# Optimization experiments

Hardware: AMD Instinct MI355X
Metric: run time of the kernel (lower is better)

Reference implementation:

```python
import jax, jax.numpy as jnp
import numpy as np

B, S, D_IN, D_EMB = 8, 2048, 512, 512

def setup_inputs() -> dict:
    key = jax.random.key(0)
    ks = jax.random.split(key, 7)
    s = 1.0 / np.sqrt(D_IN)
    return {
        "x": jax.random.normal(ks[0], (B, S, D_IN), dtype=jnp.float32),
        "Wq": jax.random.uniform(ks[1], (D_IN, D_EMB), jnp.float32, -s, s),
        "bq": jax.random.uniform(ks[2], (D_EMB,), jnp.float32, -s, s),
        "Wk": jax.random.uniform(ks[3], (D_IN, D_EMB), jnp.float32, -s, s),
        "bk": jax.random.uniform(ks[4], (D_EMB,), jnp.float32, -s, s),
        "Wv": jax.random.uniform(ks[5], (D_IN, D_EMB), jnp.float32, -s, s),
        "bv": jax.random.uniform(ks[6], (D_EMB,), jnp.float32, -s, s),
    }

def reference(x, Wq, bq, Wk, bk, Wv, bv):
    # single-head attention: softmax(QK^T / sqrt(d)) V
    q = x @ Wq + bq            # [B,S,E]
    k = x @ Wk + bk
    v = x @ Wv + bv
    scores = jnp.einsum('bse,bte->bst', q, k) / jnp.sqrt(jnp.float32(D_EMB))
    attn = jax.nn.softmax(scores, axis=-1)  # [B,S,S]
    return jnp.einsum('bst,bte->bse', attn, v)
```

## Files before the change

### kernel.cpp

```cpp
#include <hip/hip_runtime.h>
#include <stdint.h>


using f32x4 = __attribute__((ext_vector_type(4))) float;
using s16x8 = __attribute__((ext_vector_type(8))) short;
using u16x4 = __attribute__((ext_vector_type(4))) unsigned short;

#define S_LEN 2048
#define EMB   512

#define ASYNC16(g, l)                                                     \
  __builtin_amdgcn_global_load_lds(                                       \
      (const __attribute__((address_space(1))) void*)(g),                 \
      (__attribute__((address_space(3))) void*)(l), 16, 0, 0)

__device__ __forceinline__ unsigned short f2bf(float f) {
  union { float f; unsigned u; } v; v.f = f;
  unsigned r = v.u + 0x7fffu + ((v.u >> 16) & 1u);
  return (unsigned short)(r >> 16);
}

__global__ __launch_bounds__(256) void xconv_kernel(
    const float* __restrict__ x, short* __restrict__ xb) {
  int i = (blockIdx.x * 256 + threadIdx.x) * 8;
  f32x4 a = *(const f32x4*)(x + i);
  f32x4 b = *(const f32x4*)(x + i + 4);
  s16x8 h;
  h[0] = (short)f2bf(a[0]); h[1] = (short)f2bf(a[1]);
  h[2] = (short)f2bf(a[2]); h[3] = (short)f2bf(a[3]);
  h[4] = (short)f2bf(b[0]); h[5] = (short)f2bf(b[1]);
  h[6] = (short)f2bf(b[2]); h[7] = (short)f2bf(b[3]);
  *(s16x8*)(xb + i) = h;
}

__global__ __launch_bounds__(256) void wconv_kernel(
    const float* __restrict__ Wq, const float* __restrict__ Wk,
    const float* __restrict__ Wv, short* __restrict__ Wt) {
  __shared__ float T[64][65];
  int bid = blockIdx.x;
  int mat = bid >> 6;
  int t   = bid & 63;
  int k0  = (t & 7) << 6, n0 = (t >> 3) << 6;
  const float* W = (mat == 0) ? Wq : (mat == 1) ? Wk : Wv;
  int tid = threadIdx.x;
  int rr = tid >> 4, cc = tid & 15;
#pragma unroll
  for (int p = 0; p < 4; ++p) {
    int row = p * 16 + rr;
    f32x4 v = *(const f32x4*)(W + (size_t)(k0 + row) * 512 + n0 + cc * 4);
#pragma unroll
    for (int j = 0; j < 4; ++j) T[row][cc * 4 + j] = v[j];
  }
  __syncthreads();
  short* D = Wt + (size_t)mat * 262144;
#pragma unroll
  for (int p = 0; p < 4; ++p) {
    int nrow = p * 16 + rr;
    u16x4 h;
#pragma unroll
    for (int j = 0; j < 4; ++j) h[j] = f2bf(T[cc * 4 + j][nrow]);
    *(u16x4*)(D + (size_t)(n0 + nrow) * 512 + k0 + cc * 4) = h;
  }
}

__global__ __launch_bounds__(256) void qkv_gemm(
    const short* __restrict__ xb, const short* __restrict__ Wt,
    const float* __restrict__ bq, const float* __restrict__ bk,
    const float* __restrict__ bv,
    short* __restrict__ Qg, short* __restrict__ Kg, short* __restrict__ VTg) {
  __shared__ __align__(16) short As[2][128 * 64];
  __shared__ __align__(16) short Bs[2][128 * 64];
  int gid = blockIdx.x;
  int mat = gid >> 9;
  int rem = gid & 511;
  int mt  = rem & 127, nt = rem >> 7;
  int m0  = mt << 7,   n0 = nt << 7;
  const short* W    = Wt + (size_t)mat * 262144;
  const float* bias = (mat == 0) ? bq : (mat == 1) ? bk : bv;

  int tid = threadIdx.x, lane = tid & 63, wv = tid >> 6;
  int l16 = lane & 15, quad = lane >> 4;
  int wr = (wv & 1) << 6, wc = (wv >> 1) << 6;
  int drow = lane >> 3;
  int dchk = (lane & 7) ^ drow;

  const short* asrc[4];
  const short* bsrc[4];
#pragma unroll
  for (int i = 0; i < 4; ++i) {
    int row = (wv * 4 + i) * 8 + drow;
    asrc[i] = xb + (size_t)(m0 + row) * 512 + dchk * 8;
    bsrc[i] = W  + (size_t)(n0 + row) * 512 + dchk * 8;
  }

  const f32x4 Z4 = {0.f, 0.f, 0.f, 0.f};
  f32x4 acc[4][4];
#pragma unroll
  for (int a = 0; a < 4; ++a)
#pragma unroll
    for (int c = 0; c < 4; ++c) acc[a][c] = Z4;

#pragma unroll
  for (int i = 0; i < 4; ++i) {
    int g = wv * 4 + i;
    ASYNC16(asrc[i], &As[0][g * 512]);
    ASYNC16(bsrc[i], &Bs[0][g * 512]);
  }
  __syncthreads();

  for (int it = 0; it < 8; ++it) {
    int buf = it & 1;
    if (it < 7) {
      int k1 = (it + 1) << 6;
#pragma unroll
      for (int i = 0; i < 4; ++i) {
        int g = wv * 4 + i;
        ASYNC16(asrc[i] + k1, &As[buf ^ 1][g * 512]);
        ASYNC16(bsrc[i] + k1, &Bs[buf ^ 1][g * 512]);
      }
    }
#pragma unroll
    for (int kk = 0; kk < 2; ++kk) {
      s16x8 af[4], bfr[4];
#pragma unroll
      for (int rb = 0; rb < 4; ++rb) {
        int row = wr + rb * 16 + l16;
        int c   = kk * 4 + quad;
        af[rb] = *(const s16x8*)(&As[buf][row * 64 + ((c ^ (row & 7)) * 8)]);
      }
#pragma unroll
      for (int cb = 0; cb < 4; ++cb) {
        int row = wc + cb * 16 + l16;
        int c   = kk * 4 + quad;
        bfr[cb] = *(const s16x8*)(&Bs[buf][row * 64 + ((c ^ (row & 7)) * 8)]);
      }
#pragma unroll
      for (int rb = 0; rb < 4; ++rb)
#pragma unroll
        for (int cb = 0; cb < 4; ++cb)
          acc[rb][cb] = __builtin_amdgcn_mfma_f32_16x16x32_bf16(af[rb], bfr[cb], acc[rb][cb], 0, 0, 0);
    }
    __syncthreads();
  }

  float bsv[4];
#pragma unroll
  for (int cb = 0; cb < 4; ++cb) bsv[cb] = bias[n0 + wc + cb * 16 + l16];

  if (mat < 2) {
    short* D = (mat == 0) ? Qg : Kg;
#pragma unroll
    for (int rb = 0; rb < 4; ++rb)
#pragma unroll
      for (int cb = 0; cb < 4; ++cb)
#pragma unroll
        for (int r = 0; r < 4; ++r) {
          int m = m0 + wr + rb * 16 + quad * 4 + r;
          D[(size_t)m * 512 + n0 + wc + cb * 16 + l16] =
              (short)f2bf(acc[rb][cb][r] + bsv[cb]);
        }
  } else {
#pragma unroll
    for (int rb = 0; rb < 4; ++rb)
#pragma unroll
      for (int cb = 0; cb < 4; ++cb) {
        u16x4 h;
#pragma unroll
        for (int r = 0; r < 4; ++r) h[r] = f2bf(acc[rb][cb][r] + bsv[cb]);
        int m  = m0 + wr + rb * 16 + quad * 4;
        int bb = m >> 11, sl = m & 2047;
        int e  = n0 + wc + cb * 16 + l16;
        size_t idx = ((((size_t)bb * 32 + (e >> 4)) * 64 + (sl >> 5)) * 16 +
                      (e & 15)) * 32 + (sl & 31);
        *(u16x4*)(VTg + idx) = h;
      }
  }
}

__global__ __launch_bounds__(512, 2) void attn_kernel(
    const short* __restrict__ Qg, const short* __restrict__ Kg,
    const short* __restrict__ VTg, float* __restrict__ out) {
  __shared__ __align__(16) short Kt[3][32 * 512];
  __shared__ __align__(16) short Pl[2][64 * 40];
  __shared__ float l_l[64];
  const float SCL2 = 0.06375871855f;

  int b = blockIdx.x & 7, qt = blockIdx.x >> 3;
  int s0 = qt << 6;
  int tid = threadIdx.x, lane = tid & 63, wv = tid >> 6;
  int l16 = lane & 15, quad = lane >> 4;
  int a = wv & 3, h = wv >> 2;
  int e0 = wv << 6;

  const short* Kb = Kg  + (size_t)b * S_LEN * 512;
  const short* Vb = VTg + (size_t)b * 1048576;

  const short* kdma[4];
#pragma unroll
  for (int i = 0; i < 4; ++i) {
    int r = wv * 4 + i;
    kdma[i] = Kb + (size_t)r * 512 + ((lane ^ (r & 7)) * 8);
  }
  const short* vbase = Vb + (size_t)wv * 131072 + l16 * 32 + quad * 8;

#pragma unroll
  for (int i = 0; i < 4; ++i)
    ASYNC16(kdma[i], &Kt[0][(wv * 4 + i) * 512]);
#pragma unroll
  for (int i = 0; i < 4; ++i)
    ASYNC16(kdma[i] + 16384, &Kt[1][(wv * 4 + i) * 512]);

  const short* qrow = Qg + ((size_t)b * S_LEN + s0 + a * 16 + l16) * 512 + quad * 8;
  s16x8 qf[16];
#pragma unroll
  for (int kk = 0; kk < 16; ++kk) qf[kk] = *(const s16x8*)(qrow + kk * 32);

  const f32x4 Z4 = {0.f, 0.f, 0.f, 0.f};
  f32x4 acc[4][4];
#pragma unroll
  for (int rb = 0; rb < 4; ++rb)
#pragma unroll
    for (int cb = 0; cb < 4; ++cb) acc[rb][cb] = Z4;
  f32x4 lsum = Z4;

  __syncthreads();

  int rbuf = 0, wbuf = 2;
  for (int kt = 0; kt < 64; ++kt) {
    s16x8 vf[4];
#pragma unroll
    for (int cb = 0; cb < 4; ++cb)
      vf[cb] = *(const s16x8*)(vbase + (size_t)cb * 32768 + (size_t)kt * 512);
    __builtin_amdgcn_sched_barrier(0);

    {
      size_t adv = (size_t)((kt + 2) & 63) * 16384;
#pragma unroll
      for (int i = 0; i < 4; ++i)
        ASYNC16(kdma[i] + adv, &Kt[wbuf][(wv * 4 + i) * 512]);
    }
    __builtin_amdgcn_sched_barrier(0);

    f32x4 s_a = Z4, s_b = Z4;
    int krow = h * 16 + l16;
    const short* kb = &Kt[rbuf][krow * 512];
    int ksw = krow & 7;
    __builtin_amdgcn_s_setprio(1);
#pragma unroll
    for (int kk = 0; kk < 8; ++kk) {
      s16x8 kf0 = *(const s16x8*)(kb + (((2 * kk) * 4 + quad) ^ ksw) * 8);
      s_a = __builtin_amdgcn_mfma_f32_16x16x32_bf16(qf[2 * kk], kf0, s_a, 0, 0, 0);
      s16x8 kf1 = *(const s16x8*)(kb + (((2 * kk + 1) * 4 + quad) ^ ksw) * 8);
      s_b = __builtin_amdgcn_mfma_f32_16x16x32_bf16(qf[2 * kk + 1], kf1, s_b, 0, 0, 0);
    }
    __builtin_amdgcn_s_setprio(0);
    f32x4 sv = s_a + s_b;

    short* Pc = Pl[kt & 1];
#pragma unroll
    for (int r = 0; r < 4; ++r) {
      float p = exp2f(sv[r] * SCL2);
      lsum[r] += p;
      Pc[(a * 16 + quad * 4 + r) * 40 + h * 16 + l16] = (short)f2bf(p);
    }

    asm volatile("s_waitcnt vmcnt(8) lgkmcnt(0)\n\ts_barrier" ::: "memory");

    s16x8 pf[4];
#pragma unroll
    for (int g = 0; g < 4; ++g)
      pf[g] = *(const s16x8*)(Pc + (g * 16 + l16) * 40 + quad * 8);
    __builtin_amdgcn_s_setprio(1);
#pragma unroll
    for (int cb = 0; cb < 4; ++cb)
#pragma unroll
      for (int g = 0; g < 4; ++g)
        acc[g][cb] = __builtin_amdgcn_mfma_f32_16x16x32_bf16(pf[g], vf[cb], acc[g][cb], 0, 0, 0);
    __builtin_amdgcn_s_setprio(0);

    rbuf = (rbuf == 2) ? 0 : rbuf + 1;
    wbuf = (wbuf == 2) ? 0 : wbuf + 1;
  }

#pragma unroll
  for (int r = 0; r < 4; ++r) {
    float v = lsum[r];
    v += __shfl_xor(v, 1);
    v += __shfl_xor(v, 2);
    v += __shfl_xor(v, 4);
    v += __shfl_xor(v, 8);
    lsum[r] = v;
  }
  if (h == 0 && l16 == 0) {
#pragma unroll
    for (int r = 0; r < 4; ++r) l_l[a * 16 + quad * 4 + r] = lsum[r];
  }
  __syncthreads();
  if (h == 1 && l16 == 0) {
#pragma unroll
    for (int r = 0; r < 4; ++r) l_l[a * 16 + quad * 4 + r] += lsum[r];
  }
  __syncthreads();

#pragma unroll
  for (int rb = 0; rb < 4; ++rb) {
    f32x4 lv = *(const f32x4*)(l_l + rb * 16 + quad * 4);
    f32x4 li;
#pragma unroll
    for (int r = 0; r < 4; ++r) li[r] = 1.0f / lv[r];
#pragma unroll
    for (int cb = 0; cb < 4; ++cb)
#pragma unroll
      for (int r = 0; r < 4; ++r)
        out[((size_t)b * S_LEN + s0 + rb * 16 + quad * 4 + r) * 512 + e0 + cb * 16 + l16] =
            acc[rb][cb][r] * li[r];
  }
}

extern "C" void kernel_launch(void* const* d_in, const int* in_sizes, int n_in,
                              void* d_out, int out_size, void* d_ws, size_t ws_size,
                              hipStream_t stream) {
  const float* x  = (const float*)d_in[0];
  const float* Wq = (const float*)d_in[1];
  const float* bq = (const float*)d_in[2];
  const float* Wk = (const float*)d_in[3];
  const float* bk = (const float*)d_in[4];
  const float* Wv = (const float*)d_in[5];
  const float* bv = (const float*)d_in[6];

  short* Wt  = (short*)d_ws;
  short* xb  = (short*)((char*)d_ws + 1572864);
  short* Qg  = xb + (size_t)8388608;
  short* Kg  = Qg + (size_t)8388608;
  short* VTg = Kg + (size_t)8388608;

  xconv_kernel<<<4096, 256, 0, stream>>>(x, xb);
  wconv_kernel<<<192, 256, 0, stream>>>(Wq, Wk, Wv, Wt);
  qkv_gemm<<<1536, 256, 0, stream>>>(xb, Wt, bq, bk, bv, Qg, Kg, VTg);
  attn_kernel<<<256, 512, 0, stream>>>(Qg, Kg, VTg, (float*)d_out);
}
```

Before: 240.8 us.

## Warp-specialize attention kernel into QK-softmax producer and PV consumer waves

```diff
diff --git a/kernel.cpp b/kernel.cpp
--- a/kernel.cpp
+++ b/kernel.cpp
@@ -189,8 +189,6 @@
   int s0 = qt << 6;
   int tid = threadIdx.x, lane = tid & 63, wv = tid >> 6;
   int l16 = lane & 15, quad = lane >> 4;
-  int a = wv & 3, h = wv >> 2;
-  int e0 = wv << 6;
 
   const short* Kb = Kg  + (size_t)b * S_LEN * 512;
   const short* Vb = VTg + (size_t)b * 1048576;
@@ -201,7 +199,6 @@
     int r = wv * 4 + i;
     kdma[i] = Kb + (size_t)r * 512 + ((lane ^ (r & 7)) * 8);
   }
-  const short* vbase = Vb + (size_t)wv * 131072 + l16 * 32 + quad * 8;
 
 #pragma unroll
   for (int i = 0; i < 4; ++i)
@@ -210,110 +207,184 @@
   for (int i = 0; i < 4; ++i)
     ASYNC16(kdma[i] + 16384, &Kt[1][(wv * 4 + i) * 512]);
 
-  const short* qrow = Qg + ((size_t)b * S_LEN + s0 + a * 16 + l16) * 512 + quad * 8;
-  s16x8 qf[16];
-#pragma unroll
-  for (int kk = 0; kk < 16; ++kk) qf[kk] = *(const s16x8*)(qrow + kk * 32);
-
-  const f32x4 Z4 = {0.f, 0.f, 0.f, 0.f};
-  f32x4 acc[4][4];
-#pragma unroll
-  for (int rb = 0; rb < 4; ++rb)
-#pragma unroll
-    for (int cb = 0; cb < 4; ++cb) acc[rb][cb] = Z4;
-  f32x4 lsum = Z4;
-
-  __syncthreads();
-
-  int rbuf = 0, wbuf = 2;
-  for (int kt = 0; kt < 64; ++kt) {
-    s16x8 vf[4];
-#pragma unroll
-    for (int cb = 0; cb < 4; ++cb)
-      vf[cb] = *(const s16x8*)(vbase + (size_t)cb * 32768 + (size_t)kt * 512);
+  if (wv < 4) {
+    int a = wv & 1, h = wv >> 1;
+    const short* qrowA = Qg + ((size_t)b * S_LEN + s0 + a * 32 + l16) * 512 + quad * 8;
+    const short* qrowB = qrowA + (size_t)16 * 512;
+    s16x8 qfA[16], qfB[16];
+#pragma unroll
+    for (int c = 0; c < 16; ++c) {
+      qfA[c] = *(const s16x8*)(qrowA + c * 32);
+      qfB[c] = *(const s16x8*)(qrowB + c * 32);
+    }
+    const f32x4 Z4 = {0.f, 0.f, 0.f, 0.f};
+    f32x4 lsumA = Z4, lsumB = Z4;
+
+    __syncthreads();
+
+    for (int kt = 0; kt < 64; ++kt) {
+      int rbuf = kt % 3, wbuf = (kt + 2) % 3;
+      {
+        size_t adv = (size_t)((kt + 2) & 63) * 16384;
+#pragma unroll
+        for (int i = 0; i < 4; ++i)
+          ASYNC16(kdma[i] + adv, &Kt[wbuf][(wv * 4 + i) * 512]);
+      }
+      __builtin_amdgcn_sched_barrier(0);
+
+      f32x4 sA = Z4, sB = Z4;
+      int krow = h * 16 + l16;
+      const short* kb = &Kt[rbuf][krow * 512];
+      int ksw = krow & 7;
+      __builtin_amdgcn_s_setprio(1);
+#pragma unroll
+      for (int c = 0; c < 16; ++c) {
+        s16x8 kf = *(const s16x8*)(kb + (((c * 4 + quad) ^ ksw) * 8));
+        sA = __builtin_amdgcn_mfma_f32_16x16x32_bf16(qfA[c], kf, sA, 0, 0, 0);
+        sB = __builtin_amdgcn_mfma_f32_16x16x32_bf16(qfB[c], kf, sB, 0, 0, 0);
+      }
+      __builtin_amdgcn_s_setprio(0);
+
+      short* Pc = Pl[kt & 1];
+#pragma unroll
+      for (int r = 0; r < 4; ++r) {
+        float pA = exp2f(sA[r] * SCL2);
+        lsumA[r] += pA;
+        Pc[(a * 32 + quad * 4 + r) * 40 + h * 16 + l16] = (short)f2bf(pA);
+        float pB = exp2f(sB[r] * SCL2);
+        lsumB[r] += pB;
+        Pc[(a * 32 + 16 + quad * 4 + r) * 40 + h * 16 + l16] = (short)f2bf(pB);
+      }
+
+      asm volatile("s_waitcnt vmcnt(4) lgkmcnt(0)\n\ts_barrier" ::: "memory");
+      __builtin_amdgcn_sched_barrier(0);
+    }
+
+#pragma unroll
+    for (int r = 0; r < 4; ++r) {
+      float vA = lsumA[r];
+      vA += __shfl_xor(vA, 1); vA += __shfl_xor(vA, 2);
+      vA += __shfl_xor(vA, 4); vA += __shfl_xor(vA, 8);
+      lsumA[r] = vA;
+      float vB = lsumB[r];
+      vB += __shfl_xor(vB, 1); vB += __shfl_xor(vB, 2);
+      vB += __shfl_xor(vB, 4); vB += __shfl_xor(vB, 8);
+      lsumB[r] = vB;
+    }
+    if (h == 0 && l16 == 0) {
+#pragma unroll
+      for (int r = 0; r < 4; ++r) {
+        l_l[a * 32 + quad * 4 + r]      = lsumA[r];
+        l_l[a * 32 + 16 + quad * 4 + r] = lsumB[r];
+      }
+    }
+    __syncthreads();
+    if (h == 1 && l16 == 0) {
+#pragma unroll
+      for (int r = 0; r < 4; ++r) {
+        l_l[a * 32 + quad * 4 + r]      += lsumA[r];
+        l_l[a * 32 + 16 + quad * 4 + r] += lsumB[r];
+      }
+    }
+    __syncthreads();
+  } else {
+    int pw = wv - 4;
+    int e0 = pw << 7;
+    const short* vbase = Vb + (size_t)pw * 262144 + l16 * 32 + quad * 8;
+
+    const f32x4 Z4 = {0.f, 0.f, 0.f, 0.f};
+    f32x4 acc[4][8];
+#pragma unroll
+    for (int g = 0; g < 4; ++g)
+#pragma unroll
+      for (int cb = 0; cb < 8; ++cb) acc[g][cb] = Z4;
+    s16x8 vfA[8], vfB[8];
+
+    __syncthreads();
+
+    for (int kt = 0; kt < 64; kt += 2) {
+      {
+        size_t adv = (size_t)((kt + 2) & 63) * 16384;
+        int wbuf = (kt + 2) % 3;
+#pragma unroll
+        for (int i = 0; i < 4; ++i)
+          ASYNC16(kdma[i] + adv, &Kt[wbuf][(wv * 4 + i) * 512]);
+      }
+#pragma unroll
+      for (int cb = 0; cb < 8; ++cb)
+        vfA[cb] = *(const s16x8*)(vbase + (size_t)cb * 32768 + (size_t)kt * 512);
+      if (kt) {
+        s16x8 pf[4];
+#pragma unroll
+        for (int g = 0; g < 4; ++g)
+          pf[g] = *(const s16x8*)(&Pl[1][(g * 16 + l16) * 40 + quad * 8]);
+        __builtin_amdgcn_s_setprio(1);
+#pragma unroll
+        for (int cb = 0; cb < 8; ++cb)
+#pragma unroll
+          for (int g = 0; g < 4; ++g)
+            acc[g][cb] = __builtin_amdgcn_mfma_f32_16x16x32_bf16(pf[g], vfB[cb], acc[g][cb], 0, 0, 0);
+        __builtin_amdgcn_s_setprio(0);
+      }
+      asm volatile("s_waitcnt lgkmcnt(0)\n\ts_barrier" ::: "memory");
+      __builtin_amdgcn_sched_barrier(0);
+
+      {
+        size_t adv = (size_t)((kt + 3) & 63) * 16384;
+        int wbuf = (kt + 3) % 3;
+#pragma unroll
+        for (int i = 0; i < 4; ++i)
+          ASYNC16(kdma[i] + adv, &Kt[wbuf][(wv * 4 + i) * 512]);
+      }
+#pragma unroll
+      for (int cb = 0; cb < 8; ++cb)
+        vfB[cb] = *(const s16x8*)(vbase + (size_t)cb * 32768 + (size_t)(kt + 1) * 512);
+      {
+        s16x8 pf[4];
+#pragma unroll
+        for (int g = 0; g < 4; ++g)
+          pf[g] = *(const s16x8*)(&Pl[0][(g * 16 + l16) * 40 + quad * 8]);
+        __builtin_amdgcn_s_setprio(1);
+#pragma unroll
+        for (int cb = 0; cb < 8; ++cb)
+#pragma unroll
+          for (int g = 0; g < 4; ++g)
+            acc[g][cb] = __builtin_amdgcn_mfma_f32_16x16x32_bf16(pf[g], vfA[cb], acc[g][cb], 0, 0, 0);
+        __builtin_amdgcn_s_setprio(0);
+      }
+      asm volatile("s_waitcnt lgkmcnt(0)\n\ts_barrier" ::: "memory");
+      __builtin_amdgcn_sched_barrier(0);
+    }
+
+    asm volatile("s_waitcnt vmcnt(0)" ::: "memory");
     __builtin_amdgcn_sched_barrier(0);
-
     {
-      size_t adv = (size_t)((kt + 2) & 63) * 16384;
-#pragma unroll
-      for (int i = 0; i < 4; ++i)
-        ASYNC16(kdma[i] + adv, &Kt[wbuf][(wv * 4 + i) * 512]);
-    }
-    __builtin_amdgcn_sched_barrier(0);
-
-    f32x4 s_a = Z4, s_b = Z4;
-    int krow = h * 16 + l16;
-    const short* kb = &Kt[rbuf][krow * 512];
-    int ksw = krow & 7;
-    __builtin_amdgcn_s_setprio(1);
-#pragma unroll
-    for (int kk = 0; kk < 8; ++kk) {
-      s16x8 kf0 = *(const s16x8*)(kb + (((2 * kk) * 4 + quad) ^ ksw) * 8);
-      s_a = __builtin_amdgcn_mfma_f32_16x16x32_bf16(qf[2 * kk], kf0, s_a, 0, 0, 0);
-      s16x8 kf1 = *(const s16x8*)(kb + (((2 * kk + 1) * 4 + quad) ^ ksw) * 8);
-      s_b = __builtin_amdgcn_mfma_f32_16x16x32_bf16(qf[2 * kk + 1], kf1, s_b, 0, 0, 0);
-    }
-    __builtin_amdgcn_s_setprio(0);
-    f32x4 sv = s_a + s_b;
-
-    short* Pc = Pl[kt & 1];
-#pragma unroll
-    for (int r = 0; r < 4; ++r) {
-      float p = exp2f(sv[r] * SCL2);
-      lsum[r] += p;
-      Pc[(a * 16 + quad * 4 + r) * 40 + h * 16 + l16] = (short)f2bf(p);
-    }
-
-    asm volatile("s_waitcnt vmcnt(8) lgkmcnt(0)\n\ts_barrier" ::: "memory");
-
-    s16x8 pf[4];
-#pragma unroll
-    for (int g = 0; g < 4; ++g)
-      pf[g] = *(const s16x8*)(Pc + (g * 16 + l16) * 40 + quad * 8);
-    __builtin_amdgcn_s_setprio(1);
-#pragma unroll
-    for (int cb = 0; cb < 4; ++cb)
+      s16x8 pf[4];
 #pragma unroll
       for (int g = 0; g < 4; ++g)
-        acc[g][cb] = __builtin_amdgcn_mfma_f32_16x16x32_bf16(pf[g], vf[cb], acc[g][cb], 0, 0, 0);
-    __builtin_amdgcn_s_setprio(0);
-
-    rbuf = (rbuf == 2) ? 0 : rbuf + 1;
-    wbuf = (wbuf == 2) ? 0 : wbuf + 1;
-  }
-
-#pragma unroll
-  for (int r = 0; r < 4; ++r) {
-    float v = lsum[r];
-    v += __shfl_xor(v, 1);
-    v += __shfl_xor(v, 2);
-    v += __shfl_xor(v, 4);
-    v += __shfl_xor(v, 8);
-    lsum[r] = v;
-  }
-  if (h == 0 && l16 == 0) {
-#pragma unroll
-    for (int r = 0; r < 4; ++r) l_l[a * 16 + quad * 4 + r] = lsum[r];
-  }
-  __syncthreads();
-  if (h == 1 && l16 == 0) {
-#pragma unroll
-    for (int r = 0; r < 4; ++r) l_l[a * 16 + quad * 4 + r] += lsum[r];
-  }
-  __syncthreads();
-
-#pragma unroll
-  for (int rb = 0; rb < 4; ++rb) {
-    f32x4 lv = *(const f32x4*)(l_l + rb * 16 + quad * 4);
-    f32x4 li;
-#pragma unroll
-    for (int r = 0; r < 4; ++r) li[r] = 1.0f / lv[r];
-#pragma unroll
-    for (int cb = 0; cb < 4; ++cb)
-#pragma unroll
-      for (int r = 0; r < 4; ++r)
-        out[((size_t)b * S_LEN + s0 + rb * 16 + quad * 4 + r) * 512 + e0 + cb * 16 + l16] =
-            acc[rb][cb][r] * li[r];
+        pf[g] = *(const s16x8*)(&Pl[1][(g * 16 + l16) * 40 + quad * 8]);
+#pragma unroll
+      for (int cb = 0; cb < 8; ++cb)
+#pragma unroll
+        for (int g = 0; g < 4; ++g)
+          acc[g][cb] = __builtin_amdgcn_mfma_f32_16x16x32_bf16(pf[g], vfB[cb], acc[g][cb], 0, 0, 0);
+    }
+    __syncthreads();
+    __syncthreads();
+
+#pragma unroll
+    for (int g = 0; g < 4; ++g) {
+      f32x4 lv = *(const f32x4*)(l_l + g * 16 + quad * 4);
+      f32x4 li;
+#pragma unroll
+      for (int r = 0; r < 4; ++r) li[r] = 1.0f / lv[r];
+#pragma unroll
+      for (int cb = 0; cb < 8; ++cb)
+#pragma unroll
+        for (int r = 0; r < 4; ++r)
+          out[((size_t)b * S_LEN + s0 + g * 16 + quad * 4 + r) * 512 + e0 + cb * 16 + l16] =
+              acc[g][cb][r] * li[r];
+    }
   }
 }
 
```

Result: faster. 222.4 us (-7.7%).
